# Optimization experiments

Hardware: AMD Instinct MI355X
Metric: run time of the kernel (lower is better)

The kernel has to match this reference:

```python
import jax, jax.numpy as jnp
import numpy as np

HEADS = 16
HEAD_DIM = 128


def rotate_half(x):
    x1, x2 = jnp.split(x, 2, axis=-1)
    return jnp.concatenate((-x2, x1), axis=-1)


def setup_inputs() -> dict:
    key = jax.random.key(0)
    ks = jax.random.split(key, 8)
    b, s, h = 2, 2048, 2048
    x = jax.random.normal(ks[0], (b, s, h), dtype=jnp.float32)
    attention_mask = jnp.zeros((1, 1, s, s), dtype=jnp.float32)
    alibi = jax.random.normal(ks[1], (1, HEADS, 1, s), dtype=jnp.float32)
    freqs = jax.random.normal(ks[2], (1, 1, s, HEAD_DIM), dtype=jnp.float32)
    scale = 1.0 / np.sqrt(h)
    Wq = jax.random.normal(ks[3], (h, h), dtype=jnp.float32) * scale
    Wk = jax.random.normal(ks[4], (h, h), dtype=jnp.float32) * scale
    Wv = jax.random.normal(ks[5], (h, h), dtype=jnp.float32) * scale
    Wo = jax.random.normal(ks[6], (h, h), dtype=jnp.float32) * scale
    return {"x": x, "attention_mask": attention_mask, "alibi": alibi,
            "freqs": freqs, "Wq": Wq, "Wk": Wk, "Wv": Wv, "Wo": Wo}


def reference(x, attention_mask, alibi, freqs, Wq, Wk, Wv, Wo):
    b, s, hidden = x.shape
    # torch Linear: y = x @ W.T (weight shape [out, in])
    def proj(W):
        y = x @ W.T
        return y.reshape(b, s, HEADS, HEAD_DIM).transpose(0, 2, 1, 3)  # [b,H,s,d]
    q, k, v = proj(Wq), proj(Wk), proj(Wv)
    cos, sin = jnp.cos(freqs), jnp.sin(freqs)
    q = q * cos + rotate_half(q) * sin
    k = k * cos + rotate_half(k) * sin
    scores = jnp.einsum('bhqd,bhkd->bhqk', q, k) / np.sqrt(HEAD_DIM)
    scores = scores + attention_mask + alibi
    attn = jax.nn.softmax(scores, axis=-1)
    out = jnp.einsum('bhqk,bhkd->bhqd', attn, v)
    out = out.transpose(0, 2, 1, 3).reshape(b, s, hidden)
    return out @ Wo.T
```

## Files before the change

### kernel.cpp

```cpp
#include <hip/hip_runtime.h>
#include <math.h>

typedef __attribute__((ext_vector_type(8))) short short8;
typedef __attribute__((ext_vector_type(4))) float f32x4;
typedef __attribute__((ext_vector_type(4))) unsigned short us4;
typedef __attribute__((ext_vector_type(4))) float fl4;

#define B_ 2
#define S_ 2048
#define H_ 16
#define D_ 128
#define HID 2048

__device__ __forceinline__ unsigned short f2bf(float f){
  unsigned u = __builtin_bit_cast(unsigned, f);
  u += 0x7fffu + ((u >> 16) & 1u);
  return (unsigned short)(u >> 16);
}
__device__ __forceinline__ float bf2f(unsigned short u){
  unsigned x = ((unsigned)u) << 16;
  return __builtin_bit_cast(float, x);
}
__device__ __forceinline__ int cvtpk(float lo, float hi){
  int r; asm("v_cvt_pk_bf16_f32 %0, %1, %2" : "=v"(r) : "v"(lo), "v"(hi)); return r;
}

__device__ __forceinline__ void g2lds16(const unsigned short* g, unsigned short* l){
  __builtin_amdgcn_global_load_lds(
      (const __attribute__((address_space(1))) unsigned int*)g,
      (__attribute__((address_space(3))) unsigned int*)l, 16, 0, 0);
}

__global__ void cvt_k(const float* __restrict__ src, unsigned short* __restrict__ dst){
  int i = (blockIdx.x * 256 + threadIdx.x) * 4;
  fl4 v = *(const fl4*)(src + i);
  us4 o;
  #pragma unroll
  for (int t = 0; t < 4; t++) o[t] = f2bf(v[t]);
  *(us4*)(dst + i) = o;
}

__global__ void tab_k(const float* __restrict__ freqs, float* __restrict__ ctab,
                      float* __restrict__ stab){
  int i = blockIdx.x * 256 + threadIdx.x;
  float f = freqs[i];
  ctab[i] = cosf(f);
  stab[i] = sinf(f);
}

#define PHEND_VM  do { asm volatile("s_waitcnt vmcnt(6)" ::: "memory"); \
  __builtin_amdgcn_sched_barrier(0); __builtin_amdgcn_s_barrier(); } while(0)
#define PHEND     do { \
  __builtin_amdgcn_sched_barrier(0); __builtin_amdgcn_s_barrier(); } while(0)
#define PREBAR    __builtin_amdgcn_s_barrier()

#define RD_A(slotb, half) do { _Pragma("unroll") \
  for (int i = 0; i < 4; i++){ _Pragma("unroll") \
    for (int ks = 0; ks < 2; ks++) \
      a[i][ks] = *(const short8*)(L + (slotb) + (half)*8192 + abase + i*2048 + kg[ks]); } } while(0)

#define RD_B(slotb, half) do { _Pragma("unroll") \
  for (int n = 0; n < 2; n++){ _Pragma("unroll") \
    for (int ks = 0; ks < 2; ks++) \
      b[(half)*2+n][ks] = *(const short8*)(L + (slotb) + 16384 + (half)*8192 + bbase + n*4096 + kg[ks]); } } while(0)

#define MMQ(X, Y) do { __builtin_amdgcn_s_setprio(1); _Pragma("unroll") \
  for (int i = 0; i < 4; i++){ _Pragma("unroll") \
    for (int n = 0; n < 2; n++){ _Pragma("unroll") \
      for (int ks = 0; ks < 2; ks++) \
        acc[(X)*4+i][(Y)*2+n] = __builtin_amdgcn_mfma_f32_16x16x32_bf16( \
            a[i][ks], b[(Y)*2+n][ks], acc[(X)*4+i][(Y)*2+n], 0, 0, 0); } } \
  __builtin_amdgcn_s_setprio(0); } while(0)

template<int EPI>
__global__ __launch_bounds__(512, 2) void gemm8_k(
    const unsigned short* __restrict__ A,
    const unsigned short* __restrict__ W0,
    const unsigned short* __restrict__ W1,
    const unsigned short* __restrict__ W2,
    unsigned short* __restrict__ O0,
    unsigned short* __restrict__ O1,
    unsigned short* __restrict__ O2,
    float* __restrict__ Of)
{
  __shared__ __align__(16) unsigned short L[2 * 4 * 8192];
  const int tid = threadIdx.x;
  const int l = tid & 63, lg = l >> 4, lr = l & 15;
  const int w = tid >> 6, wm = w >> 2, wn = w & 3;
  const int m0 = blockIdx.x * 256, n0 = blockIdx.y * 256;
  const int z = (EPI == 1) ? blockIdx.z : 0;
  const unsigned short* Bop = (EPI == 1) ? (z == 0 ? W0 : (z == 1 ? W1 : W2)) : W0;

  f32x4 acc[8][4];
  #pragma unroll
  for (int i = 0; i < 8; i++)
    #pragma unroll
    for (int j = 0; j < 4; j++)
      acc[i][j] = f32x4{0.f, 0.f, 0.f, 0.f};

  const int gsw = (((tid & 7) ^ ((tid >> 3) & 7)) * 8);
  const unsigned short* gA = A   + (size_t)(m0 + (tid >> 3)) * HID + gsw;
  const unsigned short* gB = Bop + (size_t)(n0 + (tid >> 3)) * HID + gsw;
  const size_t HIN = (size_t)64  * HID;
  const size_t HB  = (size_t)128 * HID;

  const int abase = (wm * 16 + lr) * 64;
  const int bbase = (wn * 16 + lr) * 64;
  int kg[2];
  kg[0] = ((lg)     ^ (lr & 7)) * 8;
  kg[1] = ((4 + lg) ^ (lr & 7)) * 8;

  #define STG(gsrc, tile, ldst) do { \
    const unsigned short* _s = (gsrc) + (size_t)(tile) * 64; \
    g2lds16(_s,       (ldst) + tid * 8); \
    g2lds16(_s + HIN, (ldst) + 4096 + tid * 8); } while(0)

  short8 a[4][2], b[4][2];

  STG(gA, 0, L);
  STG(gA + HB, 0, L + 8192);
  STG(gB, 0, L + 16384);
  STG(gB + HB, 0, L + 24576);
  asm volatile("s_waitcnt vmcnt(0)" ::: "memory");
  __builtin_amdgcn_sched_barrier(0);
  __builtin_amdgcn_s_barrier();
  STG(gA, 1, L + 32768);

  for (int it = 0; it < 16; ++it){
    const int t1 = 2 * it + 1, t2 = 2 * it + 2, t3 = 2 * it + 3;
    RD_A(0, 0); RD_B(0, 0);
    STG(gB, t1, L + 32768 + 16384);
    PREBAR; MMQ(0, 0); PHEND_VM;
    RD_B(0, 1);
    STG(gB + HB, t1, L + 32768 + 24576);
    PREBAR; MMQ(0, 1); PHEND_VM;
    RD_A(0, 1);
    STG(gA + HB, t1, L + 32768 + 8192);
    PREBAR; MMQ(1, 0); PHEND;
    STG(gA, t2, L);
    PREBAR; MMQ(1, 1); PHEND_VM;
    RD_A(32768, 0); RD_B(32768, 0);
    STG(gB, t2, L + 16384);
    PREBAR; MMQ(0, 0); PHEND_VM;
    RD_B(32768, 1);
    STG(gB + HB, t2, L + 24576);
    PREBAR; MMQ(0, 1); PHEND_VM;
    RD_A(32768, 1);
    STG(gA + HB, t2, L + 8192);
    PREBAR; MMQ(1, 0); PHEND;
    STG(gA, t3, L + 32768);
    PREBAR; MMQ(1, 1); PHEND_VM;
  }
  #undef STG

  #pragma unroll
  for (int mf = 0; mf < 8; mf++)
    #pragma unroll
    for (int nf = 0; nf < 4; nf++){
      const int j = n0 + nf * 64 + wn * 16 + lr;
      const int i0 = m0 + mf * 32 + wm * 16 + lg * 4;
      if (EPI == 0){
        #pragma unroll
        for (int r = 0; r < 4; r++)
          Of[(size_t)(i0 + r) * HID + j] = acc[mf][nf][r];
      } else if (z == 2){
        const int b = i0 >> 11, s = i0 & 2047, h = j >> 7, d = j & 127;
        us4 v;
        #pragma unroll
        for (int r = 0; r < 4; r++) v[r] = f2bf(acc[mf][nf][r]);
        *(us4*)(O2 + ((size_t)(b * H_ + h) * D_ + d) * S_ + s) = v;
      } else {
        unsigned short* O = z ? O1 : O0;
        const int h = j >> 7, d = j & 127;
        #pragma unroll
        for (int r = 0; r < 4; r++){
          const int i = i0 + r;
          const int b = i >> 11, s = i & 2047;
          O[((size_t)(b * H_ + h) * S_ + s) * D_ + d] = f2bf(acc[mf][nf][r]);
        }
      }
    }
}

__global__ void rope_k(unsigned short* __restrict__ Q, unsigned short* __restrict__ K,
                       const float* __restrict__ ctab, const float* __restrict__ stab){
  int idx = blockIdx.x * 256 + threadIdx.x;
  unsigned short* P = (idx >= (1 << 20)) ? K : Q;
  int e  = idx & ((1 << 20) - 1);
  int g  = e & 15;
  int s  = (e >> 4) & 2047;
  int bh = e >> 15;
  int d0 = g * 4;
  size_t base = ((size_t)bh * S_ + s) * D_;
  us4 qa = *(us4*)(P + base + d0);
  us4 qb = *(us4*)(P + base + d0 + 64);
  fl4 ca = *(const fl4*)(ctab + s * D_ + d0);
  fl4 sa = *(const fl4*)(stab + s * D_ + d0);
  fl4 cb = *(const fl4*)(ctab + s * D_ + d0 + 64);
  fl4 sb = *(const fl4*)(stab + s * D_ + d0 + 64);
  us4 oa, ob;
  #pragma unroll
  for (int t = 0; t < 4; t++){
    float xa = bf2f(qa[t]), xb = bf2f(qb[t]);
    oa[t] = f2bf(xa * ca[t] - xb * sa[t]);
    ob[t] = f2bf(xb * cb[t] + xa * sb[t]);
  }
  *(us4*)(P + base + d0)      = oa;
  *(us4*)(P + base + d0 + 64) = ob;
}

__global__ __launch_bounds__(256) void attn_k(
    const unsigned short* __restrict__ Q,
    const unsigned short* __restrict__ Kg,
    const unsigned short* __restrict__ Vt,
    const float* __restrict__ mask,
    const float* __restrict__ alibi,
    unsigned short* __restrict__ Ctx)
{
  __shared__ __align__(16) unsigned short Kl[2][64 * 128];
  __shared__ __align__(16) unsigned short Vl[2][128 * 64];
  const int tid = threadIdx.x;
  const int l = tid & 63, lg = l >> 4, lr = l & 15;
  const int w = tid >> 6;
  const int bh = blockIdx.y, b = bh >> 4, h = bh & 15;
  const int q0 = blockIdx.x * 64 + w * 16;
  const size_t hb = (size_t)bh * S_ * D_;
  const float* mrow = mask + (size_t)(q0 + lr) * S_;
  const float* al = alibi + h * S_;
  const int sidx = (l & 48) + ((l & 48) >> 2);
  const float SCL2E = 0.08838834764831845f * 1.4426950408889634f;
  const float L2E = 1.4426950408889634f;

  const int kswz = (((tid & 15) ^ ((tid >> 4) & 7)) * 8);
  const unsigned short* gK = Kg + hb + (size_t)(tid >> 4) * D_ + kswz;
  const int vswz = (((tid & 7) ^ ((tid >> 3) & 7)) * 8);
  const unsigned short* gV = Vt + hb + (size_t)(tid >> 3) * S_ + vswz;

  #define ASTAGE(buf, kv)  do {                                            \
    g2lds16(gK + (size_t)((kv))      * D_, Kl[buf] + tid * 8);             \
    g2lds16(gK + (size_t)((kv) + 16) * D_, Kl[buf] + 2048 + tid * 8);      \
    g2lds16(gK + (size_t)((kv) + 32) * D_, Kl[buf] + 4096 + tid * 8);      \
    g2lds16(gK + (size_t)((kv) + 48) * D_, Kl[buf] + 6144 + tid * 8);      \
    g2lds16(gV + (kv),                     Vl[buf] + tid * 8);             \
    g2lds16(gV + 32 * S_ + (kv),           Vl[buf] + 2048 + tid * 8);      \
    g2lds16(gV + 64 * S_ + (kv),           Vl[buf] + 4096 + tid * 8);      \
    g2lds16(gV + 96 * S_ + (kv),           Vl[buf] + 6144 + tid * 8);      \
  } while (0)

  int koff[4];
  #pragma unroll
  for (int c = 0; c < 4; c++) koff[c] = ((c * 4 + lg) ^ (lr & 7)) * 8;
  const int vo0 = (lg ^ (lr & 7)) * 8, vo1 = ((4 + lg) ^ (lr & 7)) * 8;

  short8 qf[4];
  #pragma unroll
  for (int c = 0; c < 4; c++)
    qf[c] = *(const short8*)(Q + hb + (size_t)(q0 + lr) * D_ + c * 32 + lg * 8);

  f32x4 acc[8];
  #pragma unroll
  for (int c = 0; c < 8; c++) acc[c] = f32x4{0.f, 0.f, 0.f, 0.f};
  float mr = -1e30f, lsum = 0.f;

  ASTAGE(0, 0);
  __syncthreads();
  int cur = 0;

  for (int t = 0; t < 32; t++){
    const int kv0 = t * 64;
    if (t < 31) ASTAGE(cur ^ 1, kv0 + 64);

    fl4 mk[4], aa[4];
    #pragma unroll
    for (int g = 0; g < 4; g++){
      mk[g] = *(const fl4*)(mrow + kv0 + g * 16 + 4 * lg);
      aa[g] = *(const fl4*)(al  + kv0 + g * 16 + 4 * lg);
    }

    f32x4 sg[4];
    #pragma unroll
    for (int g = 0; g < 4; g++) sg[g] = f32x4{0.f, 0.f, 0.f, 0.f};
    #pragma unroll
    for (int g = 0; g < 4; g++){
      const int row = g * 16 + lr;
      #pragma unroll
      for (int c = 0; c < 4; c++){
        short8 kf = *(const short8*)(Kl[cur] + row * 128 + koff[c]);
        sg[g] = __builtin_amdgcn_mfma_f32_16x16x32_bf16(kf, qf[c], sg[g], 0, 0, 0);
      }
    }

    float x[4][4];
    #pragma unroll
    for (int g = 0; g < 4; g++)
      #pragma unroll
      for (int r = 0; r < 4; r++)
        x[g][r] = fmaf(sg[g][r], SCL2E, (mk[g][r] + aa[g][r]) * L2E);

    float mx = -1e30f;
    #pragma unroll
    for (int g = 0; g < 4; g++)
      #pragma unroll
      for (int r = 0; r < 4; r++) mx = fmaxf(mx, x[g][r]);

    float p[4][4], ps = 0.f;
    if (__all(mx <= mr + 8.f)){
      #pragma unroll
      for (int g = 0; g < 4; g++)
        #pragma unroll
        for (int r = 0; r < 4; r++){
          p[g][r] = exp2f(x[g][r] - mr);
          ps += p[g][r];
        }
      ps += __shfl_xor(ps, 16);
      ps += __shfl_xor(ps, 32);
      lsum += ps;
    } else {
      mx = fmaxf(mx, __shfl_xor(mx, 16));
      mx = fmaxf(mx, __shfl_xor(mx, 32));
      float mnew = fmaxf(mr, mx);
      float alpha = exp2f(mr - mnew);
      #pragma unroll
      for (int g = 0; g < 4; g++)
        #pragma unroll
        for (int r = 0; r < 4; r++){
          p[g][r] = exp2f(x[g][r] - mnew);
          ps += p[g][r];
        }
      ps += __shfl_xor(ps, 16);
      ps += __shfl_xor(ps, 32);
      lsum = lsum * alpha + ps;
      mr = mnew;
      float ar[4];
      #pragma unroll
      for (int r = 0; r < 4; r++) ar[r] = __shfl(alpha, sidx + r);
      #pragma unroll
      for (int c = 0; c < 8; c++)
        #pragma unroll
        for (int r = 0; r < 4; r++) acc[c][r] *= ar[r];
    }

    int pk0[4], pk1[4];
    #pragma unroll
    for (int r = 0; r < 4; r++){
      pk0[r] = cvtpk(p[0][r], p[1][r]);
      pk1[r] = cvtpk(p[2][r], p[3][r]);
    }

    const int srcb = lr + ((lg & 1) << 5);
    short8 af0, af1;
    #pragma unroll
    for (int j = 0; j < 8; j++){
      int w0 = __shfl(pk0[j & 3], srcb + ((j >> 2) << 4));
      int w1 = __shfl(pk1[j & 3], srcb + ((j >> 2) << 4));
      af0[j] = (short)((l & 32) ? ((unsigned)w0 >> 16) : ((unsigned)w0 & 0xffffu));
      af1[j] = (short)((l & 32) ? ((unsigned)w1 >> 16) : ((unsigned)w1 & 0xffffu));
    }

    #pragma unroll
    for (int c = 0; c < 8; c++){
      const int d0 = c * 16 + lr;
      short8 vf0 = *(const short8*)(Vl[cur] + d0 * 64 + vo0);
      short8 vf1 = *(const short8*)(Vl[cur] + d0 * 64 + vo1);
      acc[c] = __builtin_amdgcn_mfma_f32_16x16x32_bf16(af0, vf0, acc[c], 0, 0, 0);
      acc[c] = __builtin_amdgcn_mfma_f32_16x16x32_bf16(af1, vf1, acc[c], 0, 0, 0);
    }

    __syncthreads();
    cur ^= 1;
  }
  #undef ASTAGE

  float inv = 1.f / lsum;
  float ir[4];
  #pragma unroll
  for (int r = 0; r < 4; r++) ir[r] = __shfl(inv, sidx + r);
  #pragma unroll
  for (int r = 0; r < 4; r++){
    const int qg = q0 + 4 * lg + r;
    const size_t ob = ((size_t)(b * S_ + qg) * H_ + h) * D_;
    #pragma unroll
    for (int c = 0; c < 8; c++)
      Ctx[ob + c * 16 + lr] = f2bf(acc[c][r] * ir[r]);
  }
}

extern "C" void kernel_launch(void* const* d_in, const int* in_sizes, int n_in,
                              void* d_out, int out_size, void* d_ws, size_t ws_size,
                              hipStream_t stream){
  const float* x     = (const float*)d_in[0];
  const float* mask  = (const float*)d_in[1];
  const float* alibi = (const float*)d_in[2];
  const float* freqs = (const float*)d_in[3];
  const float* Wq    = (const float*)d_in[4];
  const float* Wk    = (const float*)d_in[5];
  const float* Wv    = (const float*)d_in[6];
  const float* Wo    = (const float*)d_in[7];
  float* out = (float*)d_out;

  unsigned short* ws  = (unsigned short*)d_ws;
  unsigned short* xb  = ws;
  unsigned short* wqb = ws + 8388608;
  unsigned short* wkb = ws + 12582912;
  unsigned short* wvb = ws + 16777216;
  unsigned short* wob = ws + 20971520;
  unsigned short* Qb  = ws + 25165824;
  unsigned short* Kb  = ws + 33554432;
  unsigned short* Vb  = ws + 41943040;
  unsigned short* ctx = xb;
  float* ctab = (float*)(ws + 50331648);
  float* stab = ctab + 262144;

  cvt_k<<<8192, 256, 0, stream>>>(x,  xb);
  cvt_k<<<4096, 256, 0, stream>>>(Wq, wqb);
  cvt_k<<<4096, 256, 0, stream>>>(Wk, wkb);
  cvt_k<<<4096, 256, 0, stream>>>(Wv, wvb);
  cvt_k<<<4096, 256, 0, stream>>>(Wo, wob);
  tab_k<<<1024, 256, 0, stream>>>(freqs, ctab, stab);

  gemm8_k<1><<<dim3(16, 8, 3), 512, 0, stream>>>(xb, wqb, wkb, wvb,
                                                 Qb, Kb, Vb, nullptr);
  rope_k<<<8192, 256, 0, stream>>>(Qb, Kb, ctab, stab);
  attn_k<<<dim3(32, 32), 256, 0, stream>>>(Qb, Kb, Vb, mask, alibi, ctx);
  gemm8_k<0><<<dim3(16, 8, 1), 512, 0, stream>>>(ctx, wob, nullptr, nullptr,
                                                 nullptr, nullptr, nullptr, out);
}
```

Baseline: 508.7 us.

## Shrink GEMM N-tile to 128 and rework the LDS pipeline schedule

The GEMM kernel's output tile changes from 256x256 to 256x128, with half the accumulators and a smaller LDS footprint. The grids double in y, so more blocks are available to fill the GPU's compute units. The main loop is rewritten into two phases per k-tile, with a new prefetch order, new vmcnt waits and an explicit tail. The smaller tile lowers per-block register and LDS pressure and raises parallelism, but each block reuses less data and more global traffic goes to reloading A.

After: 498.8 us. No clear change (-2.0%).

```diff
diff --git a/kernel.cpp b/kernel.cpp
--- a/kernel.cpp
+++ b/kernel.cpp
@@ -48,28 +48,26 @@
   stab[i] = sinf(f);
 }
 
-#define PHEND_VM  do { asm volatile("s_waitcnt vmcnt(6)" ::: "memory"); \
-  __builtin_amdgcn_sched_barrier(0); __builtin_amdgcn_s_barrier(); } while(0)
-#define PHEND     do { \
-  __builtin_amdgcn_sched_barrier(0); __builtin_amdgcn_s_barrier(); } while(0)
-#define PREBAR    __builtin_amdgcn_s_barrier()
-
-#define RD_A(slotb, half) do { _Pragma("unroll") \
+#define SB __builtin_amdgcn_sched_barrier(0)
+#define BAR __builtin_amdgcn_s_barrier()
+#define VM(n) asm volatile("s_waitcnt vmcnt(" #n ")" ::: "memory")
+
+#define RD_A8(slotb, half) do { _Pragma("unroll") \
   for (int i = 0; i < 4; i++){ _Pragma("unroll") \
     for (int ks = 0; ks < 2; ks++) \
       a[i][ks] = *(const short8*)(L + (slotb) + (half)*8192 + abase + i*2048 + kg[ks]); } } while(0)
 
-#define RD_B(slotb, half) do { _Pragma("unroll") \
+#define RD_B8(slotb) do { _Pragma("unroll") \
   for (int n = 0; n < 2; n++){ _Pragma("unroll") \
     for (int ks = 0; ks < 2; ks++) \
-      b[(half)*2+n][ks] = *(const short8*)(L + (slotb) + 16384 + (half)*8192 + bbase + n*4096 + kg[ks]); } } while(0)
-
-#define MMQ(X, Y) do { __builtin_amdgcn_s_setprio(1); _Pragma("unroll") \
+      b[n][ks] = *(const short8*)(L + (slotb) + 16384 + bbase + n*4096 + kg[ks]); } } while(0)
+
+#define MMQ8(X) do { __builtin_amdgcn_s_setprio(1); _Pragma("unroll") \
   for (int i = 0; i < 4; i++){ _Pragma("unroll") \
     for (int n = 0; n < 2; n++){ _Pragma("unroll") \
       for (int ks = 0; ks < 2; ks++) \
-        acc[(X)*4+i][(Y)*2+n] = __builtin_amdgcn_mfma_f32_16x16x32_bf16( \
-            a[i][ks], b[(Y)*2+n][ks], acc[(X)*4+i][(Y)*2+n], 0, 0, 0); } } \
+        acc[(X)*4+i][n] = __builtin_amdgcn_mfma_f32_16x16x32_bf16( \
+            a[i][ks], b[n][ks], acc[(X)*4+i][n], 0, 0, 0); } } \
   __builtin_amdgcn_s_setprio(0); } while(0)
 
 template<int EPI>
@@ -83,19 +81,19 @@
     unsigned short* __restrict__ O2,
     float* __restrict__ Of)
 {
-  __shared__ __align__(16) unsigned short L[2 * 4 * 8192];
+  __shared__ __align__(16) unsigned short L[2 * 3 * 8192];
   const int tid = threadIdx.x;
   const int l = tid & 63, lg = l >> 4, lr = l & 15;
   const int w = tid >> 6, wm = w >> 2, wn = w & 3;
-  const int m0 = blockIdx.x * 256, n0 = blockIdx.y * 256;
+  const int m0 = blockIdx.x * 256, n0 = blockIdx.y * 128;
   const int z = (EPI == 1) ? blockIdx.z : 0;
   const unsigned short* Bop = (EPI == 1) ? (z == 0 ? W0 : (z == 1 ? W1 : W2)) : W0;
 
-  f32x4 acc[8][4];
+  f32x4 acc[8][2];
   #pragma unroll
   for (int i = 0; i < 8; i++)
     #pragma unroll
-    for (int j = 0; j < 4; j++)
+    for (int j = 0; j < 2; j++)
       acc[i][j] = f32x4{0.f, 0.f, 0.f, 0.f};
 
   const int gsw = (((tid & 7) ^ ((tid >> 3) & 7)) * 8);
@@ -115,48 +113,40 @@
     g2lds16(_s,       (ldst) + tid * 8); \
     g2lds16(_s + HIN, (ldst) + 4096 + tid * 8); } while(0)
 
-  short8 a[4][2], b[4][2];
-
-  STG(gA, 0, L);
+  short8 a[4][2], b[2][2];
+
+  STG(gA,      0, L);
   STG(gA + HB, 0, L + 8192);
-  STG(gB, 0, L + 16384);
-  STG(gB + HB, 0, L + 24576);
-  asm volatile("s_waitcnt vmcnt(0)" ::: "memory");
-  __builtin_amdgcn_sched_barrier(0);
-  __builtin_amdgcn_s_barrier();
-  STG(gA, 1, L + 32768);
-
-  for (int it = 0; it < 16; ++it){
-    const int t1 = 2 * it + 1, t2 = 2 * it + 2, t3 = 2 * it + 3;
-    RD_A(0, 0); RD_B(0, 0);
-    STG(gB, t1, L + 32768 + 16384);
-    PREBAR; MMQ(0, 0); PHEND_VM;
-    RD_B(0, 1);
-    STG(gB + HB, t1, L + 32768 + 24576);
-    PREBAR; MMQ(0, 1); PHEND_VM;
-    RD_A(0, 1);
-    STG(gA + HB, t1, L + 32768 + 8192);
-    PREBAR; MMQ(1, 0); PHEND;
-    STG(gA, t2, L);
-    PREBAR; MMQ(1, 1); PHEND_VM;
-    RD_A(32768, 0); RD_B(32768, 0);
-    STG(gB, t2, L + 16384);
-    PREBAR; MMQ(0, 0); PHEND_VM;
-    RD_B(32768, 1);
-    STG(gB + HB, t2, L + 24576);
-    PREBAR; MMQ(0, 1); PHEND_VM;
-    RD_A(32768, 1);
-    STG(gA + HB, t2, L + 8192);
-    PREBAR; MMQ(1, 0); PHEND;
-    STG(gA, t3, L + 32768);
-    PREBAR; MMQ(1, 1); PHEND_VM;
+  STG(gB,      0, L + 16384);
+  VM(0); SB; BAR;
+
+  #define PH1(sl, osl, tn) do { \
+    RD_A8(sl, 0); RD_B8(sl); \
+    STG(gA, tn, L + (osl)); STG(gB, tn, L + (osl) + 16384); \
+    BAR; MMQ8(0); VM(4); SB; BAR; } while(0)
+  #define PH2(sl, osl, tn) do { \
+    RD_A8(sl, 1); \
+    STG(gA + HB, tn, L + (osl) + 8192); \
+    BAR; MMQ8(1); VM(2); SB; BAR; } while(0)
+
+  for (int it = 0; it < 15; ++it){
+    const int t1 = 2 * it + 1, t2 = 2 * it + 2;
+    PH1(0, 24576, t1); PH2(0, 24576, t1);
+    PH1(24576, 0, t2); PH2(24576, 0, t2);
   }
+  PH1(0, 24576, 31); PH2(0, 24576, 31);
+  RD_A8(24576, 0); RD_B8(24576);
+  BAR; MMQ8(0); VM(0); SB; BAR;
+  RD_A8(24576, 1);
+  BAR; MMQ8(1);
+  #undef PH1
+  #undef PH2
   #undef STG
 
   #pragma unroll
   for (int mf = 0; mf < 8; mf++)
     #pragma unroll
-    for (int nf = 0; nf < 4; nf++){
+    for (int nf = 0; nf < 2; nf++){
       const int j = n0 + nf * 64 + wn * 16 + lr;
       const int i0 = m0 + mf * 32 + wm * 16 + lg * 4;
       if (EPI == 0){
@@ -418,10 +408,10 @@
   cvt_k<<<4096, 256, 0, stream>>>(Wo, wob);
   tab_k<<<1024, 256, 0, stream>>>(freqs, ctab, stab);
 
-  gemm8_k<1><<<dim3(16, 8, 3), 512, 0, stream>>>(xb, wqb, wkb, wvb,
-                                                 Qb, Kb, Vb, nullptr);
+  gemm8_k<1><<<dim3(16, 16, 3), 512, 0, stream>>>(xb, wqb, wkb, wvb,
+                                                  Qb, Kb, Vb, nullptr);
   rope_k<<<8192, 256, 0, stream>>>(Qb, Kb, ctab, stab);
   attn_k<<<dim3(32, 32), 256, 0, stream>>>(Qb, Kb, Vb, mask, alibi, ctx);
-  gemm8_k<0><<<dim3(16, 8, 1), 512, 0, stream>>>(ctx, wob, nullptr, nullptr,
-                                                 nullptr, nullptr, nullptr, out);
-}
+  gemm8_k<0><<<dim3(16, 16, 1), 512, 0, stream>>>(ctx, wob, nullptr, nullptr,
+                                                  nullptr, nullptr, nullptr, out);
+}
```
